# Kernel optimization log

Measured on AMD Instinct MI355X. Metric: run time of the kernel, lower is better.

The kernel has to match this reference:

```python
import jax, jax.numpy as jnp
import numpy as np

B, C, H, W = 2, 128, 48, 48
NUM_HEADS = 8


def dct_matrix(N):
    # Orthonormal DCT-II matrix: D[k, n] = s_k * cos(pi * (n + 0.5) * k / N)
    n = np.arange(N)
    D = np.cos(np.pi * (n[None, :] + 0.5) * n[:, None] / N) * np.sqrt(2.0 / N)
    D[0] *= 1.0 / np.sqrt(2.0)
    return jnp.asarray(D, dtype=jnp.float32)


def setup_inputs() -> dict:
    key = jax.random.key(0)
    ks = jax.random.split(key, 10)
    w_scale = 1.0 / np.sqrt(C)  # kaiming-ish init for 1x1 convs
    inp = {
        "freq_feat": jax.random.normal(ks[0], (B, C, H, W), dtype=jnp.float32),
        "spatial_feat": jax.random.normal(ks[1], (B, C, H, W), dtype=jnp.float32),
        "Wq": jax.random.normal(ks[2], (C, C), dtype=jnp.float32) * w_scale,
        "bq": jnp.zeros((C,), dtype=jnp.float32),
        "Wk": jax.random.normal(ks[3], (C, C), dtype=jnp.float32) * w_scale,
        "bk": jnp.zeros((C,), dtype=jnp.float32),
        "Wv": jax.random.normal(ks[4], (C, C), dtype=jnp.float32) * w_scale,
        "bv": jnp.zeros((C,), dtype=jnp.float32),
        "Wo": jax.random.normal(ks[5], (C, C), dtype=jnp.float32) * w_scale,
        "bo": jnp.zeros((C,), dtype=jnp.float32),
    }
    return inp


def _proj(x, Wm, b):
    # 1x1 conv == channel-mixing GEMM
    return jnp.einsum('oc,bchw->bohw', Wm, x) + b[None, :, None, None]


def reference(freq_feat, spatial_feat, Wq, bq, Wk, bk, Wv, bv, Wo, bo):
    b, c, h, w = freq_feat.shape
    nh = NUM_HEADS
    d = c // nh
    L = h * w

    # 2D orthonormal DCT-II of the spatial features
    DH = dct_matrix(h)
    DW = dct_matrix(w)
    spatial_freq = jnp.einsum('hm,bcmn,wn->bchw', DH, spatial_feat, DW)

    Q = _proj(freq_feat, Wq, bq)
    K = _proj(spatial_freq, Wk, bk)
    V = _proj(spatial_freq, Wv, bv)

    # (B, C, H, W) -> (B, nh, L, d)
    def to_heads(x):
        return x.reshape(b, nh, d, L).transpose(0, 1, 3, 2)

    Qh, Kh, Vh = to_heads(Q), to_heads(K), to_heads(V)

    scale = 1.0 / np.sqrt(d)
    scores = jnp.einsum('bhld,bhsd->bhls', Qh, Kh) * scale  # (B, nh, L, L)
    attn = jax.nn.softmax(scores, axis=-1)
    out = jnp.einsum('bhls,bhsd->bhld', attn, Vh)  # (B, nh, L, d)

    out = out.transpose(0, 1, 3, 2).reshape(b, c, h, w)
    return _proj(out, Wo, bo)
```

## Files before the change

### kernel.cpp

```cpp
#include <hip/hip_runtime.h>
#include <math.h>

#define L_TOT 2304
#define C_TOT 128

typedef float v4f  __attribute__((ext_vector_type(4)));
typedef __bf16 v8bf __attribute__((ext_vector_type(8)));
typedef __bf16 v4bf __attribute__((ext_vector_type(4)));

#define MFMA_16x16x32_BF16(A, B, C) __builtin_amdgcn_mfma_f32_16x16x32_bf16((A), (B), (C), 0, 0, 0)

__device__ __forceinline__ void async_cp16(const __bf16* g, __bf16* l){
  __builtin_amdgcn_global_load_lds((const __attribute__((address_space(1))) unsigned int*)g,
                                   (__attribute__((address_space(3))) unsigned int*)l,
                                   16, 0, 0);
}

template<int MODE>
__device__ __forceinline__ void mfma_proj(const float* __restrict__ W,
                                          const float* __restrict__ bias,
                                          const float* __restrict__ Xb,
                                          float* __restrict__ Yf,
                                          __bf16* __restrict__ Yh,
                                          float scale,
                                          int n0, __bf16* Bhi, int tid){
  __bf16* Blo = Bhi + 4352;
  const int wave = tid >> 6, lane = tid & 63, qd = lane >> 4, cn = lane & 15;
  const int m0 = wave * 32;
  v8bf ahi[2][4], alo[2][4];
  #pragma unroll
  for (int rt = 0; rt < 2; rt++)
    #pragma unroll
    for (int ks = 0; ks < 4; ks++){
      const float* wp = W + (size_t)(m0 + rt * 16 + cn) * C_TOT + ks * 32 + qd * 8;
      float4 w0 = *(const float4*)wp;
      float4 w1 = *(const float4*)(wp + 4);
      float wv[8] = {w0.x, w0.y, w0.z, w0.w, w1.x, w1.y, w1.z, w1.w};
      #pragma unroll
      for (int j = 0; j < 8; j++){
        __bf16 h = (__bf16)wv[j];
        ahi[rt][ks][j] = h;
        alo[rt][ks][j] = (__bf16)(wv[j] - (float)h);
      }
    }
  {
    int k = tid >> 1, nh = tid & 1;
    const float* xp = Xb + (size_t)k * L_TOT + n0 + nh * 16;
    float4 x0 = *(const float4*)xp;
    float4 x1 = *(const float4*)(xp + 4);
    float4 x2 = *(const float4*)(xp + 8);
    float4 x3 = *(const float4*)(xp + 12);
    float xv[16] = {x0.x, x0.y, x0.z, x0.w, x1.x, x1.y, x1.z, x1.w,
                    x2.x, x2.y, x2.z, x2.w, x3.x, x3.y, x3.z, x3.w};
    #pragma unroll
    for (int i = 0; i < 16; i++){
      __bf16 h = (__bf16)xv[i];
      int row = nh * 16 + i;
      Bhi[row * 136 + k] = h;
      Blo[row * 136 + k] = (__bf16)(xv[i] - (float)h);
    }
  }
  __syncthreads();
  v4f acc[2][2];
  #pragma unroll
  for (int rt = 0; rt < 2; rt++)
    #pragma unroll
    for (int ct = 0; ct < 2; ct++) acc[rt][ct] = (v4f){0.f, 0.f, 0.f, 0.f};
  #pragma unroll
  for (int ks = 0; ks < 4; ks++){
    v8bf bhi[2], blo[2];
    #pragma unroll
    for (int ct = 0; ct < 2; ct++){
      bhi[ct] = *(const v8bf*)&Bhi[(ct * 16 + cn) * 136 + ks * 32 + qd * 8];
      blo[ct] = *(const v8bf*)&Blo[(ct * 16 + cn) * 136 + ks * 32 + qd * 8];
    }
    #pragma unroll
    for (int rt = 0; rt < 2; rt++)
      #pragma unroll
      for (int ct = 0; ct < 2; ct++){
        acc[rt][ct] = MFMA_16x16x32_BF16(ahi[rt][ks], bhi[ct], acc[rt][ct]);
        acc[rt][ct] = MFMA_16x16x32_BF16(ahi[rt][ks], blo[ct], acc[rt][ct]);
        acc[rt][ct] = MFMA_16x16x32_BF16(alo[rt][ks], bhi[ct], acc[rt][ct]);
      }
  }
  #pragma unroll
  for (int rt = 0; rt < 2; rt++){
    float bv[4];
    #pragma unroll
    for (int r = 0; r < 4; r++) bv[r] = bias[m0 + rt * 16 + qd * 4 + r];
    #pragma unroll
    for (int ct = 0; ct < 2; ct++){
      int col = n0 + ct * 16 + cn;
      if (MODE == 0){
        #pragma unroll
        for (int r = 0; r < 4; r++)
          Yf[(size_t)(m0 + rt * 16 + qd * 4 + r) * L_TOT + col] = acc[rt][ct][r] + bv[r];
      } else if (MODE == 1){
        v4bf kk;
        #pragma unroll
        for (int r = 0; r < 4; r++) kk[r] = (__bf16)((acc[rt][ct][r] + bv[r]) * scale);
        *(v4bf*)&Yh[(size_t)col * C_TOT + m0 + rt * 16 + qd * 4] = kk;
      } else {
        #pragma unroll
        for (int r = 0; r < 4; r++)
          Yh[(size_t)(m0 + rt * 16 + qd * 4 + r) * L_TOT + col] = (__bf16)(acc[rt][ct][r] + bv[r]);
      }
    }
  }
}

__global__ __launch_bounds__(256) void k_front(const float* __restrict__ spat,
                                               float* __restrict__ SF,
                                               const float* __restrict__ freq,
                                               const float* __restrict__ Wq,
                                               const float* __restrict__ bq,
                                               __bf16* __restrict__ QT){
  __shared__ __align__(16) unsigned char smraw[37632];
  int blk = blockIdx.x, tid = threadIdx.x;
  if (blk < 256){
    float* Ds  = (float*)smraw;
    float* DTs = Ds + 2352;
    float* Xs  = Ds + 4704;
    float* Ts  = Ds + 7056;
    const float* Xi = spat + (size_t)blk * 2304;
    float* Fi = SF + (size_t)blk * 2304;
    for (int i = tid; i < 2304; i += 256){
      int k = i / 48, n = i - k * 48;
      int m = ((2 * n + 1) * k) % 192;
      float v = cosf(0.032724923474893679f * (float)m) * 0.204124145231931508f;
      if (k == 0) v *= 0.707106781186547524f;
      Ds[k * 49 + n] = v;
      DTs[n * 49 + k] = v;
      Xs[k * 49 + n] = Xi[i];
    }
    __syncthreads();
    int tr = (tid >> 4) * 3, tc = (tid & 15) * 3;
    {
      float a[3][3] = {};
      for (int n = 0; n < 48; n++){
        float x0 = Xs[tr * 49 + n], x1 = Xs[(tr + 1) * 49 + n], x2 = Xs[(tr + 2) * 49 + n];
        float d0 = DTs[n * 49 + tc], d1 = DTs[n * 49 + tc + 1], d2 = DTs[n * 49 + tc + 2];
        a[0][0] += x0 * d0; a[0][1] += x0 * d1; a[0][2] += x0 * d2;
        a[1][0] += x1 * d0; a[1][1] += x1 * d1; a[1][2] += x1 * d2;
        a[2][0] += x2 * d0; a[2][1] += x2 * d1; a[2][2] += x2 * d2;
      }
      #pragma unroll
      for (int i = 0; i < 3; i++)
        #pragma unroll
        for (int j = 0; j < 3; j++)
          Ts[(tr + i) * 49 + tc + j] = a[i][j];
    }
    __syncthreads();
    {
      float c[3][3] = {};
      for (int m = 0; m < 48; m++){
        float d0 = Ds[tr * 49 + m], d1 = Ds[(tr + 1) * 49 + m], d2 = Ds[(tr + 2) * 49 + m];
        float t0 = Ts[m * 49 + tc], t1 = Ts[m * 49 + tc + 1], t2 = Ts[m * 49 + tc + 2];
        c[0][0] += d0 * t0; c[0][1] += d0 * t1; c[0][2] += d0 * t2;
        c[1][0] += d1 * t0; c[1][1] += d1 * t1; c[1][2] += d1 * t2;
        c[2][0] += d2 * t0; c[2][1] += d2 * t1; c[2][2] += d2 * t2;
      }
      #pragma unroll
      for (int i = 0; i < 3; i++)
        #pragma unroll
        for (int j = 0; j < 3; j++)
          Fi[(tr + i) * 48 + tc + j] = c[i][j];
    }
  } else {
    int idx = blk - 256;
    int b = idx / 72, n0 = (idx % 72) * 32;
    mfma_proj<1>(Wq, bq, freq + (size_t)b * C_TOT * L_TOT,
                 (float*)0, QT + (size_t)b * L_TOT * C_TOT, 1.0f, n0, (__bf16*)smraw, tid);
  }
}

__global__ __launch_bounds__(256) void k_kv(const float* __restrict__ SF,
                                            const float* __restrict__ Wk, const float* __restrict__ bk,
                                            const float* __restrict__ Wv, const float* __restrict__ bv,
                                            __bf16* __restrict__ KT, __bf16* __restrict__ Vg){
  __shared__ __align__(16) unsigned char smraw[17408];
  int b = blockIdx.z, n0 = blockIdx.x * 32;
  const float* Xb = SF + (size_t)b * C_TOT * L_TOT;
  if (blockIdx.y == 0)
    mfma_proj<1>(Wk, bk, Xb, (float*)0, KT + (size_t)b * L_TOT * C_TOT, 0.25f, n0, (__bf16*)smraw, threadIdx.x);
  else
    mfma_proj<2>(Wv, bv, Xb, (float*)0, Vg + (size_t)b * C_TOT * L_TOT, 1.0f, n0, (__bf16*)smraw, threadIdx.x);
}

__global__ __launch_bounds__(256) void k_oproj(const __bf16* __restrict__ AO,
                                               const float* __restrict__ Wo, const float* __restrict__ bo,
                                               float* __restrict__ out){
  __shared__ __align__(16) __bf16 Bs[32 * 136];
  int b = blockIdx.y, n0 = blockIdx.x * 32;
  int tid = threadIdx.x;
  const int wave = tid >> 6, lane = tid & 63, qd = lane >> 4, cn = lane & 15;
  const int m0 = wave * 32;
  v8bf ahi[2][4], alo[2][4];
  #pragma unroll
  for (int rt = 0; rt < 2; rt++)
    #pragma unroll
    for (int ks = 0; ks < 4; ks++){
      const float* wp = Wo + (size_t)(m0 + rt * 16 + cn) * C_TOT + ks * 32 + qd * 8;
      float4 w0 = *(const float4*)wp;
      float4 w1 = *(const float4*)(wp + 4);
      float wv[8] = {w0.x, w0.y, w0.z, w0.w, w1.x, w1.y, w1.z, w1.w};
      #pragma unroll
      for (int j = 0; j < 8; j++){
        __bf16 h = (__bf16)wv[j];
        ahi[rt][ks][j] = h;
        alo[rt][ks][j] = (__bf16)(wv[j] - (float)h);
      }
    }
  {
    int k = tid >> 1, nh = tid & 1;
    const __bf16* src = AO + ((size_t)b * C_TOT + k) * L_TOT + n0 + nh * 16;
    v8bf x0 = *(const v8bf*)src;
    v8bf x1 = *(const v8bf*)(src + 8);
    #pragma unroll
    for (int i = 0; i < 8; i++){
      Bs[(nh * 16 + i) * 136 + k] = x0[i];
      Bs[(nh * 16 + 8 + i) * 136 + k] = x1[i];
    }
  }
  __syncthreads();
  v4f acc[2][2];
  #pragma unroll
  for (int rt = 0; rt < 2; rt++)
    #pragma unroll
    for (int ct = 0; ct < 2; ct++) acc[rt][ct] = (v4f){0.f, 0.f, 0.f, 0.f};
  #pragma unroll
  for (int ks = 0; ks < 4; ks++){
    v8bf bf[2];
    #pragma unroll
    for (int ct = 0; ct < 2; ct++)
      bf[ct] = *(const v8bf*)&Bs[(ct * 16 + cn) * 136 + ks * 32 + qd * 8];
    #pragma unroll
    for (int rt = 0; rt < 2; rt++)
      #pragma unroll
      for (int ct = 0; ct < 2; ct++){
        acc[rt][ct] = MFMA_16x16x32_BF16(ahi[rt][ks], bf[ct], acc[rt][ct]);
        acc[rt][ct] = MFMA_16x16x32_BF16(alo[rt][ks], bf[ct], acc[rt][ct]);
      }
  }
  float* ob = out + (size_t)b * C_TOT * L_TOT;
  #pragma unroll
  for (int rt = 0; rt < 2; rt++){
    float bv[4];
    #pragma unroll
    for (int r = 0; r < 4; r++) bv[r] = bo[m0 + rt * 16 + qd * 4 + r];
    #pragma unroll
    for (int ct = 0; ct < 2; ct++){
      int col = n0 + ct * 16 + cn;
      #pragma unroll
      for (int r = 0; r < 4; r++)
        ob[(size_t)(m0 + rt * 16 + qd * 4 + r) * L_TOT + col] = acc[rt][ct][r] + bv[r];
    }
  }
}

__global__ __launch_bounds__(256) void k_attn(const __bf16* __restrict__ QT,
                                              const __bf16* __restrict__ KT,
                                              const __bf16* __restrict__ V,
                                              __bf16* __restrict__ AO){
  const int L = L_TOT;
  int bh = blockIdx.y;
  int b = bh >> 3, h = bh & 7;
  int c0 = h * 16;
  const __bf16* QTb = QT + (size_t)b * L * C_TOT;
  const __bf16* KTb = KT + (size_t)b * L * C_TOT;
  const __bf16* Vb  = V  + ((size_t)b * C_TOT + c0) * L;
  int tid = threadIdx.x;
  int wave = tid >> 6, lane = tid & 63;
  int qd = lane >> 4, cn = lane & 15;
  int l0 = blockIdx.x * 64;

  __shared__ __align__(16) __bf16 smem[8192 + 8192 + 2560];
  __bf16* Kt  = smem;
  __bf16* Vs  = smem + 8192;
  __bf16* Ptw = smem + 16384 + wave * 640;

  v8bf qf[4];
  #pragma unroll
  for (int t = 0; t < 4; t++){
    #pragma unroll
    for (int j = 0; j < 8; j++) qf[t][j] = (__bf16)0.0f;
  }
  if (qd < 2){
    #pragma unroll
    for (int t = 0; t < 4; t++)
      qf[t] = *(const v8bf*)&QTb[(size_t)(l0 + t * 16 + cn) * C_TOT + c0 + qd * 8];
  }

  v4f acc[4];
  float den[4] = {0.f, 0.f, 0.f, 0.f};
  #pragma unroll
  for (int t = 0; t < 4; t++) acc[t] = (v4f){0.f, 0.f, 0.f, 0.f};

  for (int ch = 0; ch < 5; ch++){
    int s0 = ch * 512;
    int cnt = (ch == 4) ? 256 : 512;
    __syncthreads();
    {
      int per = (cnt >> 5) >> 2;
      for (int jj = 0; jj < per; jj++){
        int j = wave * per + jj;
        int s = j * 32 + (lane >> 1);
        async_cp16(KTb + (size_t)(s0 + s) * C_TOT + c0 + (lane & 1) * 8,
                   Kt + j * 512);
      }
      if (cnt == 512){
        #pragma unroll
        for (int jj = 0; jj < 4; jj++){
          int d = wave * 4 + jj;
          async_cp16(Vb + (size_t)d * L + s0 + ((lane ^ (d & 7)) << 3),
                     Vs + d * 512);
        }
      } else {
        int d = tid >> 4, og = tid & 15;
        const __bf16* gp = Vb + (size_t)d * L + s0 + og * 16;
        v8bf v0 = *(const v8bf*)gp;
        v8bf v1 = *(const v8bf*)(gp + 8);
        int pd = d & 7;
        *(v8bf*)&Vs[d * 512 + (((og * 2)     ^ pd) << 3)] = v0;
        *(v8bf*)&Vs[d * 512 + (((og * 2 + 1) ^ pd) << 3)] = v1;
      }
    }
    __syncthreads();

    int nsu = cnt >> 7;
    int wbase = wave * (cnt >> 2);
    for (int su = 0; su < nsu; su++){
      int sb = wbase + su * 32;
      v8bf a0, a1;
      #pragma unroll
      for (int j = 0; j < 8; j++){ a0[j] = (__bf16)0.0f; a1[j] = (__bf16)0.0f; }
      if (qd < 2){
        a0 = *(const v8bf*)&Kt[(sb + cn) * 16 + qd * 8];
        a1 = *(const v8bf*)&Kt[(sb + 16 + cn) * 16 + qd * 8];
      }
      int jv = sb >> 3;
      v8bf vf = *(const v8bf*)&Vs[cn * 512 + (((jv + qd) ^ (cn & 7)) << 3)];
      #pragma unroll
      for (int t = 0; t < 4; t++){
        v4f z = {0.f, 0.f, 0.f, 0.f};
        v4f st0 = MFMA_16x16x32_BF16(a0, qf[t], z);
        v4f st1 = MFMA_16x16x32_BF16(a1, qf[t], z);
        float p0[4], p1[4];
        #pragma unroll
        for (int i = 0; i < 4; i++){
          p0[i] = __expf(st0[i]); den[t] += p0[i];
          p1[i] = __expf(st1[i]); den[t] += p1[i];
        }
        v4bf w0, w1;
        #pragma unroll
        for (int i = 0; i < 4; i++){ w0[i] = (__bf16)p0[i]; w1[i] = (__bf16)p1[i]; }
        *(v4bf*)&Ptw[cn * 40 + qd * 4]      = w0;
        *(v4bf*)&Ptw[cn * 40 + 16 + qd * 4] = w1;
        v8bf pf = *(const v8bf*)&Ptw[cn * 40 + qd * 8];
        acc[t] = MFMA_16x16x32_BF16(vf, pf, acc[t]);
      }
    }
  }

  __syncthreads();
  float* redA = (float*)smem;
  float* redD = (float*)(smem + 8192);
  #pragma unroll
  for (int t = 0; t < 4; t++){
    *(v4f*)&redA[((wave * 4 + t) * 64 + lane) * 4] = acc[t];
    redD[(wave * 4 + t) * 64 + lane] = den[t];
  }
  __syncthreads();
  {
    int t = wave;
    v4f a = (v4f){0.f, 0.f, 0.f, 0.f};
    float dn = 0.f;
    #pragma unroll
    for (int w2 = 0; w2 < 4; w2++){
      v4f xx = *(const v4f*)&redA[((w2 * 4 + t) * 64 + lane) * 4];
      a[0] += xx[0]; a[1] += xx[1]; a[2] += xx[2]; a[3] += xx[3];
      dn += redD[(w2 * 4 + t) * 64 + lane];
    }
    dn += __shfl_xor(dn, 16);
    dn += __shfl_xor(dn, 32);
    float inv = 1.0f / dn;
    __bf16* Ao = AO + ((size_t)b * C_TOT + c0) * L;
    #pragma unroll
    for (int r2 = 0; r2 < 4; r2++)
      Ao[(size_t)(qd * 4 + r2) * L + l0 + t * 16 + cn] = (__bf16)(a[r2] * inv);
  }
}

extern "C" void kernel_launch(void* const* d_in, const int* in_sizes, int n_in,
                              void* d_out, int out_size, void* d_ws, size_t ws_size,
                              hipStream_t stream){
  const float* freq = (const float*)d_in[0];
  const float* spat = (const float*)d_in[1];
  const float* Wq = (const float*)d_in[2]; const float* bq = (const float*)d_in[3];
  const float* Wk = (const float*)d_in[4]; const float* bk = (const float*)d_in[5];
  const float* Wv = (const float*)d_in[6]; const float* bv = (const float*)d_in[7];
  const float* Wo = (const float*)d_in[8]; const float* bo = (const float*)d_in[9];
  float* ws = (float*)d_ws;

  float* SF   = ws;
  __bf16* QTg = (__bf16*)(ws + 589824);
  __bf16* AOg = (__bf16*)(ws + 884736);
  __bf16* KTg = (__bf16*)(ws + 1179648);
  __bf16* Vg  = (__bf16*)(ws + 1474560);
  float* out = (float*)d_out;

  k_front<<<dim3(400), dim3(256), 0, stream>>>(spat, SF, freq, Wq, bq, QTg);
  k_kv<<<dim3(72, 2, 2), dim3(256), 0, stream>>>(SF, Wk, bk, Wv, bv, KTg, Vg);
  k_attn<<<dim3(36, 16), dim3(256), 0, stream>>>(QTg, KTg, Vg, AOg);
  k_oproj<<<dim3(72, 2), dim3(256), 0, stream>>>(AOg, Wo, bo, out);
}
```

Baseline: 124.6 us.

## Project K/V before DCT, use bf16 MFMA DCT, and fold log2e into scale

The change uses the fact that the 1x1 projection and the 2D DCT commute. It now projects the raw spatial features to K and V first, in one merged QKV projection kernel, then applies the DCT per channel with bf16 MFMA. That second kernel also adds the bias and writes the transposed K and the V layouts. The fp32 scalar DCT kernel and the fp32 intermediate buffer are gone. The K scale now includes log2(e), so attention can call the hardware exp2. In exchange the DCT is done in bf16 and the intermediate K and V are stored in bf16, which costs some accuracy.

```diff
diff --git a/kernel.cpp b/kernel.cpp
--- a/kernel.cpp
+++ b/kernel.cpp
@@ -3,6 +3,13 @@
 
 #define L_TOT 2304
 #define C_TOT 128
+#define KSCALE 0.36067376022224085f
+
+#if __has_builtin(__builtin_amdgcn_exp2f)
+#define EXP2(x) __builtin_amdgcn_exp2f(x)
+#else
+#define EXP2(x) __expf(0.69314718055994531f * (x))
+#endif
 
 typedef float v4f  __attribute__((ext_vector_type(4)));
 typedef __bf16 v8bf __attribute__((ext_vector_type(8)));
@@ -20,9 +27,8 @@
 __device__ __forceinline__ void mfma_proj(const float* __restrict__ W,
                                           const float* __restrict__ bias,
                                           const float* __restrict__ Xb,
-                                          float* __restrict__ Yf,
                                           __bf16* __restrict__ Yh,
-                                          float scale,
+                                          float scale, float bscale,
                                           int n0, __bf16* Bhi, int tid){
   __bf16* Blo = Bhi + 4352;
   const int wave = tid >> 6, lane = tid & 63, qd = lane >> 4, cn = lane & 15;
@@ -87,15 +93,11 @@
   for (int rt = 0; rt < 2; rt++){
     float bv[4];
     #pragma unroll
-    for (int r = 0; r < 4; r++) bv[r] = bias[m0 + rt * 16 + qd * 4 + r];
+    for (int r = 0; r < 4; r++) bv[r] = bias[m0 + rt * 16 + qd * 4 + r] * bscale;
     #pragma unroll
     for (int ct = 0; ct < 2; ct++){
       int col = n0 + ct * 16 + cn;
-      if (MODE == 0){
-        #pragma unroll
-        for (int r = 0; r < 4; r++)
-          Yf[(size_t)(m0 + rt * 16 + qd * 4 + r) * L_TOT + col] = acc[rt][ct][r] + bv[r];
-      } else if (MODE == 1){
+      if (MODE == 1){
         v4bf kk;
         #pragma unroll
         for (int r = 0; r < 4; r++) kk[r] = (__bf16)((acc[rt][ct][r] + bv[r]) * scale);
@@ -109,151 +111,96 @@
   }
 }
 
-__global__ __launch_bounds__(256) void k_front(const float* __restrict__ spat,
-                                               float* __restrict__ SF,
-                                               const float* __restrict__ freq,
-                                               const float* __restrict__ Wq,
-                                               const float* __restrict__ bq,
-                                               __bf16* __restrict__ QT){
-  __shared__ __align__(16) unsigned char smraw[37632];
+__global__ __launch_bounds__(256) void k_qkv(
+    const float* __restrict__ freq, const float* __restrict__ spat,
+    const float* __restrict__ Wq, const float* __restrict__ bq,
+    const float* __restrict__ Wk, const float* __restrict__ bk,
+    const float* __restrict__ Wv, const float* __restrict__ bv,
+    __bf16* __restrict__ QT, __bf16* __restrict__ Kraw, __bf16* __restrict__ Vraw){
+  __shared__ __align__(16) unsigned char smraw[17408];
+  int job = blockIdx.x / 144;
+  int idx = blockIdx.x % 144;
+  int b = idx / 72, n0 = (idx % 72) * 32;
+  size_t off = (size_t)b * C_TOT * L_TOT;
+  if (job == 0)
+    mfma_proj<1>(Wq, bq, freq + off, QT + (size_t)b * L_TOT * C_TOT, 1.0f, 1.0f, n0, (__bf16*)smraw, threadIdx.x);
+  else if (job == 1)
+    mfma_proj<2>(Wk, bk, spat + off, Kraw + off, 1.0f, 0.0f, n0, (__bf16*)smraw, threadIdx.x);
+  else
+    mfma_proj<2>(Wv, bv, spat + off, Vraw + off, 1.0f, 0.0f, n0, (__bf16*)smraw, threadIdx.x);
+}
+
+__global__ __launch_bounds__(256) void k_dct_kv(const __bf16* __restrict__ Kraw,
+                                                const __bf16* __restrict__ Vraw,
+                                                const float* __restrict__ bk,
+                                                const float* __restrict__ bv,
+                                                __bf16* __restrict__ KT,
+                                                __bf16* __restrict__ Vg){
+  __shared__ __align__(16) __bf16 Xs[3456];
+  __shared__ __align__(16) __bf16 Dm[3456];
+  __shared__ __align__(16) __bf16 Tt[3456];
   int blk = blockIdx.x, tid = threadIdx.x;
-  if (blk < 256){
-    float* Ds  = (float*)smraw;
-    float* DTs = Ds + 2352;
-    float* Xs  = Ds + 4704;
-    float* Ts  = Ds + 7056;
-    const float* Xi = spat + (size_t)blk * 2304;
-    float* Fi = SF + (size_t)blk * 2304;
-    for (int i = tid; i < 2304; i += 256){
-      int k = i / 48, n = i - k * 48;
-      int m = ((2 * n + 1) * k) % 192;
-      float v = cosf(0.032724923474893679f * (float)m) * 0.204124145231931508f;
-      if (k == 0) v *= 0.707106781186547524f;
-      Ds[k * 49 + n] = v;
-      DTs[n * 49 + k] = v;
-      Xs[k * 49 + n] = Xi[i];
-    }
-    __syncthreads();
-    int tr = (tid >> 4) * 3, tc = (tid & 15) * 3;
-    {
-      float a[3][3] = {};
-      for (int n = 0; n < 48; n++){
-        float x0 = Xs[tr * 49 + n], x1 = Xs[(tr + 1) * 49 + n], x2 = Xs[(tr + 2) * 49 + n];
-        float d0 = DTs[n * 49 + tc], d1 = DTs[n * 49 + tc + 1], d2 = DTs[n * 49 + tc + 2];
-        a[0][0] += x0 * d0; a[0][1] += x0 * d1; a[0][2] += x0 * d2;
-        a[1][0] += x1 * d0; a[1][1] += x1 * d1; a[1][2] += x1 * d2;
-        a[2][0] += x2 * d0; a[2][1] += x2 * d1; a[2][2] += x2 * d2;
-      }
-      #pragma unroll
-      for (int i = 0; i < 3; i++)
-        #pragma unroll
-        for (int j = 0; j < 3; j++)
-          Ts[(tr + i) * 49 + tc + j] = a[i][j];
-    }
-    __syncthreads();
-    {
-      float c[3][3] = {};
-      for (int m = 0; m < 48; m++){
-        float d0 = Ds[tr * 49 + m], d1 = Ds[(tr + 1) * 49 + m], d2 = Ds[(tr + 2) * 49 + m];
-        float t0 = Ts[m * 49 + tc], t1 = Ts[m * 49 + tc + 1], t2 = Ts[m * 49 + tc + 2];
-        c[0][0] += d0 * t0; c[0][1] += d0 * t1; c[0][2] += d0 * t2;
-        c[1][0] += d1 * t0; c[1][1] += d1 * t1; c[1][2] += d1 * t2;
-        c[2][0] += d2 * t0; c[2][1] += d2 * t1; c[2][2] += d2 * t2;
-      }
-      #pragma unroll
-      for (int i = 0; i < 3; i++)
-        #pragma unroll
-        for (int j = 0; j < 3; j++)
-          Fi[(tr + i) * 48 + tc + j] = c[i][j];
-    }
-  } else {
-    int idx = blk - 256;
-    int b = idx / 72, n0 = (idx % 72) * 32;
-    mfma_proj<1>(Wq, bq, freq + (size_t)b * C_TOT * L_TOT,
-                 (float*)0, QT + (size_t)b * L_TOT * C_TOT, 1.0f, n0, (__bf16*)smraw, tid);
-  }
-}
-
-__global__ __launch_bounds__(256) void k_kv(const float* __restrict__ SF,
-                                            const float* __restrict__ Wk, const float* __restrict__ bk,
-                                            const float* __restrict__ Wv, const float* __restrict__ bv,
-                                            __bf16* __restrict__ KT, __bf16* __restrict__ Vg){
-  __shared__ __align__(16) unsigned char smraw[17408];
-  int b = blockIdx.z, n0 = blockIdx.x * 32;
-  const float* Xb = SF + (size_t)b * C_TOT * L_TOT;
-  if (blockIdx.y == 0)
-    mfma_proj<1>(Wk, bk, Xb, (float*)0, KT + (size_t)b * L_TOT * C_TOT, 0.25f, n0, (__bf16*)smraw, threadIdx.x);
-  else
-    mfma_proj<2>(Wv, bv, Xb, (float*)0, Vg + (size_t)b * C_TOT * L_TOT, 1.0f, n0, (__bf16*)smraw, threadIdx.x);
-}
-
-__global__ __launch_bounds__(256) void k_oproj(const __bf16* __restrict__ AO,
-                                               const float* __restrict__ Wo, const float* __restrict__ bo,
-                                               float* __restrict__ out){
-  __shared__ __align__(16) __bf16 Bs[32 * 136];
-  int b = blockIdx.y, n0 = blockIdx.x * 32;
-  int tid = threadIdx.x;
-  const int wave = tid >> 6, lane = tid & 63, qd = lane >> 4, cn = lane & 15;
-  const int m0 = wave * 32;
-  v8bf ahi[2][4], alo[2][4];
-  #pragma unroll
-  for (int rt = 0; rt < 2; rt++)
-    #pragma unroll
-    for (int ks = 0; ks < 4; ks++){
-      const float* wp = Wo + (size_t)(m0 + rt * 16 + cn) * C_TOT + ks * 32 + qd * 8;
-      float4 w0 = *(const float4*)wp;
-      float4 w1 = *(const float4*)(wp + 4);
-      float wv[8] = {w0.x, w0.y, w0.z, w0.w, w1.x, w1.y, w1.z, w1.w};
-      #pragma unroll
-      for (int j = 0; j < 8; j++){
-        __bf16 h = (__bf16)wv[j];
-        ahi[rt][ks][j] = h;
-        alo[rt][ks][j] = (__bf16)(wv[j] - (float)h);
-      }
-    }
-  {
-    int k = tid >> 1, nh = tid & 1;
-    const __bf16* src = AO + ((size_t)b * C_TOT + k) * L_TOT + n0 + nh * 16;
-    v8bf x0 = *(const v8bf*)src;
-    v8bf x1 = *(const v8bf*)(src + 8);
-    #pragma unroll
-    for (int i = 0; i < 8; i++){
-      Bs[(nh * 16 + i) * 136 + k] = x0[i];
-      Bs[(nh * 16 + 8 + i) * 136 + k] = x1[i];
-    }
-  }
-  __syncthreads();
-  v4f acc[2][2];
-  #pragma unroll
-  for (int rt = 0; rt < 2; rt++)
-    #pragma unroll
-    for (int ct = 0; ct < 2; ct++) acc[rt][ct] = (v4f){0.f, 0.f, 0.f, 0.f};
-  #pragma unroll
-  for (int ks = 0; ks < 4; ks++){
-    v8bf bf[2];
-    #pragma unroll
-    for (int ct = 0; ct < 2; ct++)
-      bf[ct] = *(const v8bf*)&Bs[(ct * 16 + cn) * 136 + ks * 32 + qd * 8];
-    #pragma unroll
-    for (int rt = 0; rt < 2; rt++)
-      #pragma unroll
-      for (int ct = 0; ct < 2; ct++){
-        acc[rt][ct] = MFMA_16x16x32_BF16(ahi[rt][ks], bf[ct], acc[rt][ct]);
-        acc[rt][ct] = MFMA_16x16x32_BF16(alo[rt][ks], bf[ct], acc[rt][ct]);
-      }
-  }
-  float* ob = out + (size_t)b * C_TOT * L_TOT;
-  #pragma unroll
-  for (int rt = 0; rt < 2; rt++){
-    float bv[4];
-    #pragma unroll
-    for (int r = 0; r < 4; r++) bv[r] = bo[m0 + rt * 16 + qd * 4 + r];
-    #pragma unroll
-    for (int ct = 0; ct < 2; ct++){
-      int col = n0 + ct * 16 + cn;
-      #pragma unroll
-      for (int r = 0; r < 4; r++)
-        ob[(size_t)(m0 + rt * 16 + qd * 4 + r) * L_TOT + col] = acc[rt][ct][r] + bv[r];
+  int isV = blk >> 8;
+  int img = blk & 255;
+  int b = img >> 7, c = img & 127;
+  const __bf16* src = (isV ? Vraw : Kraw) + (size_t)img * 2304;
+  float bias = (isV ? bv : bk)[c];
+  for (int i = tid; i < 1728; i += 256){
+    ((unsigned int*)Xs)[i] = 0u;
+    ((unsigned int*)Dm)[i] = 0u;
+    ((unsigned int*)Tt)[i] = 0u;
+  }
+  __syncthreads();
+  for (int i = tid; i < 2304; i += 256){
+    int a = i / 48, n = i - a * 48;
+    int m = ((2 * n + 1) * a) % 192;
+    float v = cosf(0.032724923474893679f * (float)m) * 0.204124145231931508f;
+    if (a == 0) v *= 0.707106781186547524f;
+    Dm[a * 72 + n] = (__bf16)v;
+  }
+  for (int t = tid; t < 288; t += 256){
+    int m = t / 6, j = t - m * 6;
+    *(v8bf*)&Xs[m * 72 + j * 8] = *(const v8bf*)(src + t * 8);
+  }
+  __syncthreads();
+  int wave = tid >> 6, lane = tid & 63, qd = lane >> 4, cn = lane & 15;
+  for (int t = wave; t < 9; t += 4){
+    int mi = t / 3, wi = t - mi * 3;
+    v8bf a0 = *(const v8bf*)&Xs[(mi * 16 + cn) * 72 + qd * 8];
+    v8bf a1 = *(const v8bf*)&Xs[(mi * 16 + cn) * 72 + 32 + qd * 8];
+    v8bf b0 = *(const v8bf*)&Dm[(wi * 16 + cn) * 72 + qd * 8];
+    v8bf b1 = *(const v8bf*)&Dm[(wi * 16 + cn) * 72 + 32 + qd * 8];
+    v4f acc = (v4f){0.f, 0.f, 0.f, 0.f};
+    acc = MFMA_16x16x32_BF16(a0, b0, acc);
+    acc = MFMA_16x16x32_BF16(a1, b1, acc);
+    v4bf w4;
+    #pragma unroll
+    for (int r = 0; r < 4; r++) w4[r] = (__bf16)acc[r];
+    *(v4bf*)&Tt[(wi * 16 + cn) * 72 + mi * 16 + qd * 4] = w4;
+  }
+  __syncthreads();
+  for (int t = wave; t < 9; t += 4){
+    int hi = t / 3, wi = t - hi * 3;
+    v8bf a0 = *(const v8bf*)&Dm[(hi * 16 + cn) * 72 + qd * 8];
+    v8bf a1 = *(const v8bf*)&Dm[(hi * 16 + cn) * 72 + 32 + qd * 8];
+    v8bf b0 = *(const v8bf*)&Tt[(wi * 16 + cn) * 72 + qd * 8];
+    v8bf b1 = *(const v8bf*)&Tt[(wi * 16 + cn) * 72 + 32 + qd * 8];
+    v4f acc = (v4f){0.f, 0.f, 0.f, 0.f};
+    acc = MFMA_16x16x32_BF16(a0, b0, acc);
+    acc = MFMA_16x16x32_BF16(a1, b1, acc);
+    int w = wi * 16 + cn;
+    if (!isV){
+      #pragma unroll
+      for (int r = 0; r < 4; r++){
+        int l = (hi * 16 + qd * 4 + r) * 48 + w;
+        KT[((size_t)b * L_TOT + l) * C_TOT + c] = (__bf16)((acc[r] + bias) * KSCALE);
+      }
+    } else {
+      #pragma unroll
+      for (int r = 0; r < 4; r++){
+        int l = (hi * 16 + qd * 4 + r) * 48 + w;
+        Vg[(size_t)img * 2304 + l] = (__bf16)(acc[r] + bias);
+      }
     }
   }
 }
@@ -348,8 +295,8 @@
         float p0[4], p1[4];
         #pragma unroll
         for (int i = 0; i < 4; i++){
-          p0[i] = __expf(st0[i]); den[t] += p0[i];
-          p1[i] = __expf(st1[i]); den[t] += p1[i];
+          p0[i] = EXP2(st0[i]); den[t] += p0[i];
+          p1[i] = EXP2(st1[i]); den[t] += p1[i];
         }
         v4bf w0, w1;
         #pragma unroll
@@ -388,6 +335,77 @@
     #pragma unroll
     for (int r2 = 0; r2 < 4; r2++)
       Ao[(size_t)(qd * 4 + r2) * L + l0 + t * 16 + cn] = (__bf16)(a[r2] * inv);
+  }
+}
+
+__global__ __launch_bounds__(256) void k_oproj(const __bf16* __restrict__ AO,
+                                               const float* __restrict__ Wo, const float* __restrict__ bo,
+                                               float* __restrict__ out){
+  __shared__ __align__(16) __bf16 Bs[32 * 136];
+  int b = blockIdx.y, n0 = blockIdx.x * 32;
+  int tid = threadIdx.x;
+  const int wave = tid >> 6, lane = tid & 63, qd = lane >> 4, cn = lane & 15;
+  const int m0 = wave * 32;
+  v8bf ahi[2][4], alo[2][4];
+  #pragma unroll
+  for (int rt = 0; rt < 2; rt++)
+    #pragma unroll
+    for (int ks = 0; ks < 4; ks++){
+      const float* wp = Wo + (size_t)(m0 + rt * 16 + cn) * C_TOT + ks * 32 + qd * 8;
+      float4 w0 = *(const float4*)wp;
+      float4 w1 = *(const float4*)(wp + 4);
+      float wv[8] = {w0.x, w0.y, w0.z, w0.w, w1.x, w1.y, w1.z, w1.w};
+      #pragma unroll
+      for (int j = 0; j < 8; j++){
+        __bf16 h = (__bf16)wv[j];
+        ahi[rt][ks][j] = h;
+        alo[rt][ks][j] = (__bf16)(wv[j] - (float)h);
+      }
+    }
+  {
+    int k = tid >> 1, nh = tid & 1;
+    const __bf16* src = AO + ((size_t)b * C_TOT + k) * L_TOT + n0 + nh * 16;
+    v8bf x0 = *(const v8bf*)src;
+    v8bf x1 = *(const v8bf*)(src + 8);
+    #pragma unroll
+    for (int i = 0; i < 8; i++){
+      Bs[(nh * 16 + i) * 136 + k] = x0[i];
+      Bs[(nh * 16 + 8 + i) * 136 + k] = x1[i];
+    }
+  }
+  __syncthreads();
+  v4f acc[2][2];
+  #pragma unroll
+  for (int rt = 0; rt < 2; rt++)
+    #pragma unroll
+    for (int ct = 0; ct < 2; ct++) acc[rt][ct] = (v4f){0.f, 0.f, 0.f, 0.f};
+  #pragma unroll
+  for (int ks = 0; ks < 4; ks++){
+    v8bf bf[2];
+    #pragma unroll
+    for (int ct = 0; ct < 2; ct++)
+      bf[ct] = *(const v8bf*)&Bs[(ct * 16 + cn) * 136 + ks * 32 + qd * 8];
+    #pragma unroll
+    for (int rt = 0; rt < 2; rt++)
+      #pragma unroll
+      for (int ct = 0; ct < 2; ct++){
+        acc[rt][ct] = MFMA_16x16x32_BF16(ahi[rt][ks], bf[ct], acc[rt][ct]);
+        acc[rt][ct] = MFMA_16x16x32_BF16(alo[rt][ks], bf[ct], acc[rt][ct]);
+      }
+  }
+  float* ob = out + (size_t)b * C_TOT * L_TOT;
+  #pragma unroll
+  for (int rt = 0; rt < 2; rt++){
+    float bv[4];
+    #pragma unroll
+    for (int r = 0; r < 4; r++) bv[r] = bo[m0 + rt * 16 + qd * 4 + r];
+    #pragma unroll
+    for (int ct = 0; ct < 2; ct++){
+      int col = n0 + ct * 16 + cn;
+      #pragma unroll
+      for (int r = 0; r < 4; r++)
+        ob[(size_t)(m0 + rt * 16 + qd * 4 + r) * L_TOT + col] = acc[rt][ct][r] + bv[r];
+    }
   }
 }
 
@@ -400,17 +418,19 @@
   const float* Wk = (const float*)d_in[4]; const float* bk = (const float*)d_in[5];
   const float* Wv = (const float*)d_in[6]; const float* bv = (const float*)d_in[7];
   const float* Wo = (const float*)d_in[8]; const float* bo = (const float*)d_in[9];
-  float* ws = (float*)d_ws;
-
-  float* SF   = ws;
-  __bf16* QTg = (__bf16*)(ws + 589824);
-  __bf16* AOg = (__bf16*)(ws + 884736);
-  __bf16* KTg = (__bf16*)(ws + 1179648);
-  __bf16* Vg  = (__bf16*)(ws + 1474560);
+  __bf16* base = (__bf16*)d_ws;
+
+  __bf16* QTg  = base;
+  __bf16* Kraw = base + 589824;
+  __bf16* Vraw = base + 1179648;
+  __bf16* KTg  = base + 1769472;
+  __bf16* Vg   = base + 2359296;
+  __bf16* AOg  = base + 2949120;
   float* out = (float*)d_out;
 
-  k_front<<<dim3(400), dim3(256), 0, stream>>>(spat, SF, freq, Wq, bq, QTg);
-  k_kv<<<dim3(72, 2, 2), dim3(256), 0, stream>>>(SF, Wk, bk, Wv, bv, KTg, Vg);
+  k_qkv<<<dim3(432), dim3(256), 0, stream>>>(freq, spat, Wq, bq, Wk, bk, Wv, bv,
+                                             QTg, Kraw, Vraw);
+  k_dct_kv<<<dim3(512), dim3(256), 0, stream>>>(Kraw, Vraw, bk, bv, KTg, Vg);
   k_attn<<<dim3(36, 16), dim3(256), 0, stream>>>(QTg, KTg, Vg, AOg);
   k_oproj<<<dim3(72, 2), dim3(256), 0, stream>>>(AOg, Wo, bo, out);
 }
```

Measured after the change: 121.8 us. 1.02x faster.
